# Kernel optimization log

Measured on AMD Instinct MI355X. Metric: run time of the kernel, lower is better.

## Reference

```python
import jax, jax.numpy as jnp
import numpy as np

N, L, S = 2, 3000, 3000
C = 256          # in_depth
H = 256          # hidden_depth
FC = 8           # heads_count
SC_HID = H // FC # per-head dim of projected features
SCALE = (C // FC) ** 0.5  # torch code uses sc = in_depth // heads_count for scaling


def setup_inputs() -> dict:
    key = jax.random.key(0)
    ks = jax.random.split(key, 7)
    x0 = jax.random.normal(ks[0], (N, L, C), jnp.float32)
    x1 = jax.random.normal(ks[1], (N, S, C), jnp.float32)
    mask = jax.random.bernoulli(ks[2], 0.9, (N, L, S))
    W_proj = jax.random.normal(ks[3], (C, 2 * H), jnp.float32) / np.sqrt(C).astype(np.float32)
    b_proj = jax.random.normal(ks[4], (2 * H,), jnp.float32) * 0.01
    W_merge = jax.random.normal(ks[5], (H, C), jnp.float32) / np.sqrt(H).astype(np.float32)
    b_merge = jax.random.normal(ks[6], (C,), jnp.float32) * 0.01
    return {"x0": x0, "x1": x1, "mask": mask,
            "W_proj": W_proj, "b_proj": b_proj,
            "W_merge": W_merge, "b_merge": b_merge}


def _split_heads(x, W_proj, b_proj):
    # x: [n, t, C] -> proj [n, t, 2H] -> (qk, v) each [n, fc, t, sc]
    n, t, _ = x.shape
    p = (x @ W_proj + b_proj).reshape(n, t, 2, FC, SC_HID)  # layout (k fc sc)
    qk = jnp.transpose(p[:, :, 0], (0, 2, 1, 3))
    v = jnp.transpose(p[:, :, 1], (0, 2, 1, 3))
    return qk, v


def reference(x0, x1, mask, W_proj, b_proj, W_merge, b_merge):
    q0, v0 = _split_heads(x0, W_proj, b_proj)  # [n, f, l, d]
    q1, v1 = _split_heads(x1, W_proj, b_proj)  # [n, f, s, d]

    sim = jnp.einsum('nfld,nfsd->nfls', q0, q1)            # full score matrix
    sim = jnp.where(mask[:, None], sim, -jnp.inf) / SCALE  # mask then scale (as in torch)

    a01 = jnp.nan_to_num(jax.nn.softmax(sim, axis=3))  # rows over s
    a10 = jnp.nan_to_num(jax.nn.softmax(sim, axis=2))  # rows over l (== softmax(sim^T, -1))

    m0 = jnp.einsum('nfls,nfsd->nfld', a01, v1)  # [n, f, l, d]
    m1 = jnp.einsum('nfls,nfld->nfsd', a10, v0)  # [n, f, s, d]

    m0 = jnp.transpose(m0, (0, 2, 1, 3)).reshape(m0.shape[0], L, H) @ W_merge + b_merge
    m1 = jnp.transpose(m1, (0, 2, 1, 3)).reshape(m1.shape[0], S, H) @ W_merge + b_merge
    return m0, m1
```

## Files before the change

### kernel.cpp

```cpp
#include <hip/hip_runtime.h>
#include <cstdint>
#include <cstddef>

typedef unsigned int u32;
typedef unsigned short u16;
typedef uint8_t u8;
typedef unsigned long long u64;

constexpr int kNB = 2, kL = 3000, kS = 3000, kC = 256, kH = 256, kFC = 8, kD = 32;
constexpr int kTP = 3008;
constexpr int kMW = 48;
constexpr float kQSC = 0.5050097568f;

typedef __attribute__((ext_vector_type(8))) short short8;
typedef __attribute__((ext_vector_type(4))) float f32x4;

__device__ __forceinline__ u16 f2bf(float f) {
  u32 u = __float_as_uint(f);
  u += 0x7FFFu + ((u >> 16) & 1u);
  return (u16)(u >> 16);
}
__device__ __forceinline__ float bf2f(u16 h) { return __uint_as_float(((u32)h) << 16); }
__device__ __forceinline__ f32x4 mfma16(short8 a, short8 b, f32x4 c) {
  return __builtin_amdgcn_mfma_f32_16x16x32_bf16(a, b, c, 0, 0, 0);
}
__device__ __forceinline__ u32 pk2(float a, float b) {
  return (__float_as_uint(a) >> 16) | (__float_as_uint(b) & 0xFFFF0000u);
}
__device__ __forceinline__ float truncbf(float a) {
  return __uint_as_float(__float_as_uint(a) & 0xFFFF0000u);
}
__device__ __forceinline__ u32 bytes_nz(u32 w) {
  return ((w & 0xFFu) ? 1u : 0u) | (((w >> 8) & 0xFFu) ? 2u : 0u)
       | (((w >> 16) & 0xFFu) ? 4u : 0u) | ((w >> 24) ? 8u : 0u);
}
__device__ __forceinline__ u32 h2_nz(u32 w) {
  return ((w & 0xFFFFu) ? 1u : 0u) | ((w >> 16) ? 2u : 0u);
}

__device__ __forceinline__ u32 detect_mf_block(const u8* __restrict__ mraw,
                                               int tid, int* cnt) {
  if (tid < 8) cnt[tid] = 0;
  __syncthreads();
  uint4 mv = ((const uint4*)mraw)[tid];
  u32 wds[4] = {mv.x, mv.y, mv.z, mv.w};
  int l1[4] = {0,0,0,0}; int l3f1 = 0, l3c = 0;
#pragma unroll
  for (int k = 0; k < 4; ++k) {
    u32 wv = wds[k];
#pragma unroll
    for (int j = 0; j < 4; ++j) {
      u32 b = (wv >> (8 * j)) & 0xFFu;
      l1[j] += (b == 1u);
      if (j == 1) l3f1 += (b == 0x3Fu);
      if (j & 1) l3c += (b == 0x3Cu);
    }
  }
  if (l1[0]) atomicAdd(&cnt[0], l1[0]);
  if (l1[1]) atomicAdd(&cnt[1], l1[1]);
  if (l1[2]) atomicAdd(&cnt[2], l1[2]);
  if (l1[3]) atomicAdd(&cnt[3], l1[3]);
  if (l3f1)  atomicAdd(&cnt[4], l3f1);
  if (l3c)   atomicAdd(&cnt[5], l3c);
  __syncthreads();
  u32 mf;
  if (cnt[1] + cnt[2] + cnt[3] > 64) mf = 0;
  else if (cnt[0] > 64)              mf = 2;
  else if (cnt[4] > 64)              mf = 1;
  else if (cnt[5] > 64)              mf = 4;
  else                               mf = 3;
  return mf;
}
__device__ __forceinline__ u32 detect_f2_block(const u8* __restrict__ xraw,
                                               int tid, int* cnt) {
  if (tid == 0) cnt[0] = 0;
  __syncthreads();
  uint4 xv = ((const uint4*)xraw)[tid];
  u32 wds[4] = {xv.x, xv.y, xv.z, xv.w};
  int lex = 0;
#pragma unroll
  for (int k = 0; k < 4; ++k) {
    u32 b = (wds[k] >> 8) & 0x7Fu;
    lex += (b >= 0x3Eu && b <= 0x40u);
  }
  if (lex) atomicAdd(&cnt[0], lex);
  __syncthreads();
  return (cnt[0] > 300) ? 0u : 1u;
}

constexpr size_t SZ_Q   = (size_t)kNB * kFC * kTP * kD * 2;
constexpr size_t SZ_MH  = (size_t)kNB * kTP * kH * 2;
constexpr size_t SZ_XB  = (size_t)kNB * kL * kC * 2;
constexpr size_t SZ_MKB = (size_t)kNB * kMW * kTP * 8;
constexpr size_t OFF_Q0 = 256;
constexpr size_t OFF_Q1 = OFF_Q0 + SZ_Q;
constexpr size_t OFF_V0 = OFF_Q1 + SZ_Q;
constexpr size_t OFF_V1 = OFF_V0 + SZ_Q;
constexpr size_t OFF_M0 = OFF_V1 + SZ_Q;
constexpr size_t OFF_M1 = OFF_M0 + SZ_MH;
constexpr size_t OFF_WT = OFF_M1 + SZ_MH;
constexpr size_t OFF_WM = OFF_WT + (size_t)2 * kH * kC * 2;
constexpr size_t OFF_X0 = OFF_WM + (size_t)kC * kH * 2;
constexpr size_t OFF_X1 = OFF_X0 + SZ_XB;
constexpr size_t OFF_MKB  = OFF_X1 + SZ_XB;
constexpr size_t OFF_MKBT = OFF_MKB + SZ_MKB;

constexpr int NB_MASK = 47 * 47 * 2;
constexpr int NB_CVT  = 3000;
constexpr int NB_WT   = 2 * kH + kC;

__global__ __launch_bounds__(256) void k_prep(const void* __restrict__ mraw,
                                              const void* __restrict__ x0,
                                              const void* __restrict__ x1,
                                              const void* __restrict__ Wp,
                                              const void* __restrict__ Wm,
                                              u64* __restrict__ mkb, u64* __restrict__ mkbt,
                                              u16* __restrict__ xb0, u16* __restrict__ xb1,
                                              u16* __restrict__ WT, u16* __restrict__ WmT) {
  const int bx = blockIdx.x, tid = threadIdx.x;
  __shared__ int dcnt[8];
  if (bx < NB_MASK) {
    const u32 mf = detect_mf_block((const u8*)mraw, tid, dcnt);
    const int n = bx / 2209, r2 = bx % 2209;
    const int l0 = (r2 / 47) * 64, s0 = (r2 % 47) * 64;
    __shared__ u16 tb[64][4];
    {
      const int row = tid >> 2, sg = (tid & 3) * 16;
      const int l = l0 + row;
      u32 bits = 0;
      if (l < kL) {
        const size_t base = ((size_t)n * kL + l) * kS + s0 + sg;
        const bool full = (s0 + sg + 16 <= kS);
        if (mf == 3) {
          if (full) {
            const float4* p = (const float4*)(((const float*)mraw) + base);
            float4 a = p[0], b = p[1], c = p[2], d = p[3];
            bits = (u32)(a.x != 0.f)        | ((u32)(a.y != 0.f) << 1)
                 | ((u32)(a.z != 0.f) << 2) | ((u32)(a.w != 0.f) << 3)
                 | ((u32)(b.x != 0.f) << 4) | ((u32)(b.y != 0.f) << 5)
                 | ((u32)(b.z != 0.f) << 6) | ((u32)(b.w != 0.f) << 7)
                 | ((u32)(c.x != 0.f) << 8) | ((u32)(c.y != 0.f) << 9)
                 | ((u32)(c.z != 0.f) << 10)| ((u32)(c.w != 0.f) << 11)
                 | ((u32)(d.x != 0.f) << 12)| ((u32)(d.y != 0.f) << 13)
                 | ((u32)(d.z != 0.f) << 14)| ((u32)(d.w != 0.f) << 15);
          } else {
            for (int i = 0; i < 16; ++i)
              if (s0 + sg + i < kS && ((const float*)mraw)[base + i] != 0.f) bits |= 1u << i;
          }
        } else if (mf == 2) {
          if (full) {
            const uint4* p = (const uint4*)(((const u32*)mraw) + base);
            uint4 a = p[0], b = p[1], c = p[2], d = p[3];
            bits = (u32)(a.x != 0)        | ((u32)(a.y != 0) << 1)
                 | ((u32)(a.z != 0) << 2) | ((u32)(a.w != 0) << 3)
                 | ((u32)(b.x != 0) << 4) | ((u32)(b.y != 0) << 5)
                 | ((u32)(b.z != 0) << 6) | ((u32)(b.w != 0) << 7)
                 | ((u32)(c.x != 0) << 8) | ((u32)(c.y != 0) << 9)
                 | ((u32)(c.z != 0) << 10)| ((u32)(c.w != 0) << 11)
                 | ((u32)(d.x != 0) << 12)| ((u32)(d.y != 0) << 13)
                 | ((u32)(d.z != 0) << 14)| ((u32)(d.w != 0) << 15);
          } else {
            for (int i = 0; i < 16; ++i)
              if (s0 + sg + i < kS && ((const u32*)mraw)[base + i]) bits |= 1u << i;
          }
        } else if (mf == 0) {
          if (full) {
            const u8* m8 = (const u8*)mraw + base;
            uint2 a = *(const uint2*)(m8);
            uint2 b = *(const uint2*)(m8 + 8);
            bits = bytes_nz(a.x) | (bytes_nz(a.y) << 4)
                 | (bytes_nz(b.x) << 8) | (bytes_nz(b.y) << 12);
          } else {
            for (int i = 0; i < 16; ++i)
              if (s0 + sg + i < kS && ((const u8*)mraw)[base + i]) bits |= 1u << i;
          }
        } else {
          if (full) {
            const u16* m16 = (const u16*)mraw + base;
            uint4 a = *(const uint4*)(m16);
            uint4 b = *(const uint4*)(m16 + 8);
            bits = h2_nz(a.x) | (h2_nz(a.y) << 2) | (h2_nz(a.z) << 4) | (h2_nz(a.w) << 6)
                 | (h2_nz(b.x) << 8) | (h2_nz(b.y) << 10)
                 | (h2_nz(b.z) << 12) | (h2_nz(b.w) << 14);
          } else {
            for (int i = 0; i < 16; ++i)
              if (s0 + sg + i < kS && ((const u16*)mraw)[base + i]) bits |= 1u << i;
          }
        }
      }
      tb[row][tid & 3] = (u16)bits;
    }
    __syncthreads();
    const int w = tid >> 6, lane = tid & 63;
    for (int k = 0; k < 16; ++k) {
      const int ro = w * 16 + k;
      u32 b1 = (tb[ro][lane >> 4] >> (lane & 15)) & 1;
      u64 word = __ballot((int)b1);
      if (lane == 0) mkb[((size_t)n * kMW + (s0 >> 6)) * kTP + l0 + ro] = word;
      u32 b2 = (tb[lane][ro >> 4] >> (ro & 15)) & 1;
      u64 wordt = __ballot((int)b2);
      if (lane == 0) mkbt[((size_t)n * kMW + (l0 >> 6)) * kTP + s0 + ro] = wordt;
    }
  } else if (bx < NB_MASK + NB_CVT) {
    const u32 f2 = detect_f2_block((const u8*)x0, tid, dcnt);
    const int b2 = bx - NB_MASK;
    const void* X = (b2 >= 1500) ? x1 : x0;
    u16* B = (b2 >= 1500) ? xb1 : xb0;
    const int i = (b2 % 1500) * 256 + tid;
    if (f2 == 0) {
      ((uint2*)B)[i] = ((const uint2*)X)[i];
    } else {
      float4 v = ((const float4*)X)[i];
      uint2 o;
      o.x = (u32)f2bf(v.x) | ((u32)f2bf(v.y) << 16);
      o.y = (u32)f2bf(v.z) | ((u32)f2bf(v.w) << 16);
      ((uint2*)B)[i] = o;
    }
  } else {
    const u32 f2 = detect_f2_block((const u8*)x0, tid, dcnt);
    const int b = bx - NB_MASK - NB_CVT, k = tid;
    if (b < 2 * kH) {
      int col = b;
      u16 v = (f2 == 0) ? ((const u16*)Wp)[(size_t)k * (2 * kH) + col]
                        : f2bf(((const float*)Wp)[(size_t)k * (2 * kH) + col]);
      WT[(size_t)col * kC + k] = v;
    } else {
      int col = b - 2 * kH;
      u16 v = (f2 == 0) ? ((const u16*)Wm)[(size_t)k * kC + col]
                        : f2bf(((const float*)Wm)[(size_t)k * kC + col]);
      WmT[(size_t)col * kH + k] = v;
    }
  }
}

__global__ __launch_bounds__(256) void k_proj(const u16* __restrict__ xb0,
                                              const u16* __restrict__ xb1,
                                              const u16* __restrict__ WT,
                                              const void* __restrict__ bias,
                                              const void* __restrict__ x0raw,
                                              u16* __restrict__ q0, u16* __restrict__ v0t,
                                              u16* __restrict__ q1, u16* __restrict__ v1t) {
  __shared__ int dcnt[8];
  const int tid = threadIdx.x;
  const u32 f2 = detect_f2_block((const u8*)x0raw, tid, dcnt);
  const int z = blockIdx.z;
  const u16* X = z ? xb1 : xb0;
  u16* Q = z ? q1 : q0;
  u16* V = z ? v1t : v0t;
  const int w = tid >> 6, lane = tid & 63;
  const int quad = lane >> 4, c16 = lane & 15;
  const int rb = blockIdx.x, cb = blockIdx.y;

  __align__(16) __shared__ u16 sB[64 * 264];
  {
    const u16* wp = WT + (size_t)(cb * 64 + (tid >> 2)) * kC + (tid & 3) * 64;
    u16* sp = sB + (tid >> 2) * 264 + (tid & 3) * 64;
#pragma unroll
    for (int i = 0; i < 8; ++i) *(uint4*)(sp + i * 8) = *(const uint4*)(wp + i * 8);
  }
  __syncthreads();

  const int arow = rb * 64 + w * 16 + c16;
  const u16* ap = X + (size_t)arow * kC + quad * 8;
  f32x4 acc[4];
#pragma unroll
  for (int cg = 0; cg < 4; ++cg) acc[cg] = f32x4{0.f,0.f,0.f,0.f};
#pragma unroll
  for (int k0 = 0; k0 < 8; ++k0) {
    short8 a = *(const short8*)(ap + k0 * 32);
#pragma unroll
    for (int cg = 0; cg < 4; ++cg) {
      short8 b = *(const short8*)(sB + (cg * 16 + c16) * 264 + k0 * 32 + quad * 8);
      acc[cg] = mfma16(a, b, acc[cg]);
    }
  }

  const int row0 = rb * 64 + w * 16 + quad * 4;
  if (row0 < 6000) {
    const int n = (row0 >= kL) ? 1 : 0;
    const int t0 = row0 - n * kL;
#pragma unroll
    for (int cg = 0; cg < 4; ++cg) {
      const int c = cb * 64 + cg * 16 + c16;
      float bb = (f2 == 0) ? bf2f(((const u16*)bias)[c]) : ((const float*)bias)[c];
      if (c < kH) {
        int ff = c >> 5, d = c & 31;
        u16* qp = Q + ((size_t)(n * kFC + ff) * kTP + t0) * kD + d;
#pragma unroll
        for (int r = 0; r < 4; ++r) qp[(size_t)r * kD] = f2bf((acc[cg][r] + bb) * kQSC);
      } else {
        int cc = c - kH;
        int ff = cc >> 5, d = cc & 31;
        uint2 o;
        o.x = (u32)f2bf(acc[cg][0] + bb) | ((u32)f2bf(acc[cg][1] + bb) << 16);
        o.y = (u32)f2bf(acc[cg][2] + bb) | ((u32)f2bf(acc[cg][3] + bb) << 16);
        *(uint2*)(V + ((size_t)(n * kFC + ff) * kD + d) * kTP + t0) = o;
      }
    }
  }
}

__global__ __launch_bounds__(256) void k_flash(const u16* __restrict__ q0,
                                               const u16* __restrict__ q1,
                                               const u16* __restrict__ v0t,
                                               const u16* __restrict__ v1t,
                                               const u64* __restrict__ mkb,
                                               const u64* __restrict__ mkbt,
                                               u16* __restrict__ m0h, u16* __restrict__ m1h) {
  const int z = blockIdx.z;
  const u16* QA = z ? q1 : q0;
  const u16* QB = z ? q0 : q1;
  const u16* VT = z ? v0t : v1t;
  const u64* MB = z ? mkbt : mkb;
  u16* MO = z ? m1h : m0h;

  const int nf = blockIdx.y, n = nf >> 3, f = nf & 7;
  const int tid = threadIdx.x, w = tid >> 6, lane = tid & 63;
  const int quad = lane >> 4, c16 = lane & 15;

  __align__(16) __shared__ u16 sPall[4 * 4704];
  u16* sP = sPall + w * 4704;

  const u16* qa = QA + (size_t)(n * kFC + f) * kTP * kD;
  const u16* qb = QB + (size_t)(n * kFC + f) * kTP * kD;
  const u16* vt = VT + (size_t)(n * kFC + f) * kD * kTP;
  const u64* mb = MB + (size_t)n * kMW * kTP;

  const int l0 = blockIdx.x * 64;

  short8 af[4];
#pragma unroll
  for (int g = 0; g < 4; ++g) {
    const int ra = l0 + g * 16 + c16;
    af[g] = *(const short8*)(qa + (size_t)ra * kD + quad * 8);
  }

  f32x4 acc[4][2];
  float pSum[4];
#pragma unroll
  for (int g = 0; g < 4; ++g) {
    acc[g][0] = f32x4{0.f,0.f,0.f,0.f};
    acc[g][1] = f32x4{0.f,0.f,0.f,0.f};
    pSum[g] = 0.f;
  }

  u64 mword = mb[(size_t)w * kTP + l0 + lane];
  short8 aq0, aq1, aq2, aq3;
  {
    const u16* qbase = qb + (size_t)(w * 64 + c16) * kD + quad * 8;
    aq0 = *(const short8*)(qbase);
    aq1 = *(const short8*)(qbase + (size_t)16 * kD);
    aq2 = *(const short8*)(qbase + (size_t)32 * kD);
    aq3 = *(const short8*)(qbase + (size_t)48 * kD);
  }

#pragma unroll 1
  for (int jc = w; jc < 47; jc += 4) {
    const int j0 = jc * 64;
    const u16* vb = vt + (size_t)c16 * kTP + j0 + quad * 8;
    short8 bv00 = *(const short8*)(vb);
    short8 bv01 = *(const short8*)(vb + (size_t)16 * kTP);
    short8 bv10 = *(const short8*)(vb + 32);
    short8 bv11 = *(const short8*)(vb + (size_t)16 * kTP + 32);

    const u32 mlo = (u32)mword, mhi = (u32)(mword >> 32);

#pragma unroll
    for (int g = 0; g < 4; ++g) {
      const u32 lo = (u32)__shfl((int)mlo, g * 16 + c16);
      const u32 hi = (u32)__shfl((int)mhi, g * 16 + c16);
      float ps = 0.f;
#pragma unroll
      for (int t = 0; t < 4; ++t) {
        short8 aq = (t == 0) ? aq0 : (t == 1) ? aq1 : (t == 2) ? aq2 : aq3;
        f32x4 zz = {0.f,0.f,0.f,0.f};
        f32x4 s = mfma16(aq, af[g], zz);
        const u32 hh = (t & 2) ? hi : lo;
        const int base = (t & 1) * 16 + quad * 4;
        float p0 = ((hh >> (base + 0)) & 1) ? __builtin_amdgcn_exp2f(s[0]) : 0.f;
        float p1 = ((hh >> (base + 1)) & 1) ? __builtin_amdgcn_exp2f(s[1]) : 0.f;
        float p2 = ((hh >> (base + 2)) & 1) ? __builtin_amdgcn_exp2f(s[2]) : 0.f;
        float p3 = ((hh >> (base + 3)) & 1) ? __builtin_amdgcn_exp2f(s[3]) : 0.f;
        ps += (truncbf(p0) + truncbf(p1)) + (truncbf(p2) + truncbf(p3));
        uint2 pw; pw.x = pk2(p0, p1); pw.y = pk2(p2, p3);
        *(uint2*)(sP + (g * 16 + c16) * 72 + t * 16 + quad * 4) = pw;
      }
      pSum[g] += ps;
    }

    {
      int jn = jc + 4;
      const int jl = (jn < 47) ? jn : w;
      mword = mb[(size_t)jl * kTP + l0 + lane];
      const u16* qn = qb + (size_t)(jl * 64 + c16) * kD + quad * 8;
      aq0 = *(const short8*)(qn);
      aq1 = *(const short8*)(qn + (size_t)16 * kD);
      aq2 = *(const short8*)(qn + (size_t)32 * kD);
      aq3 = *(const short8*)(qn + (size_t)48 * kD);
    }

#pragma unroll
    for (int g = 0; g < 4; ++g) {
      short8 ap0 = *(const short8*)(sP + (g * 16 + c16) * 72 + quad * 8);
      short8 ap1 = *(const short8*)(sP + (g * 16 + c16) * 72 + 32 + quad * 8);
      acc[g][0] = mfma16(ap0, bv00, acc[g][0]);
      acc[g][1] = mfma16(ap0, bv01, acc[g][1]);
      acc[g][0] = mfma16(ap1, bv10, acc[g][0]);
      acc[g][1] = mfma16(ap1, bv11, acc[g][1]);
    }
  }

#pragma unroll
  for (int g = 0; g < 4; ++g) {
    float s = pSum[g];
    s += __shfl_xor(s, 16);
    s += __shfl_xor(s, 32);
    pSum[g] = s;
  }

  __syncthreads();
  float* buf = (float*)sPall;
  if (w > 0) {
    const int rbase = (w - 1) * 2304;
#pragma unroll
    for (int g = 0; g < 4; ++g) {
#pragma unroll
      for (int r = 0; r < 4; ++r) {
        buf[rbase + (g * 9 + r)     * 64 + lane] = acc[g][0][r];
        buf[rbase + (g * 9 + 4 + r) * 64 + lane] = acc[g][1][r];
      }
      buf[rbase + (g * 9 + 8) * 64 + lane] = pSum[g];
    }
  }
  __syncthreads();
  if (w == 0) {
#pragma unroll
    for (int g = 0; g < 4; ++g) {
      float lsum = pSum[g];
#pragma unroll
      for (int ww = 0; ww < 3; ++ww) lsum += buf[ww * 2304 + (g * 9 + 8) * 64 + lane];
#pragma unroll
      for (int r = 0; r < 4; ++r) {
        float n0 = acc[g][0][r], n1 = acc[g][1][r];
#pragma unroll
        for (int ww = 0; ww < 3; ++ww) {
          n0 += buf[ww * 2304 + (g * 9 + r)     * 64 + lane];
          n1 += buf[ww * 2304 + (g * 9 + 4 + r) * 64 + lane];
        }
        float ls = __shfl(lsum, quad * 4 + r);
        float rd = (ls > 0.f) ? (1.f / ls) : 0.f;
        int lrow = l0 + g * 16 + quad * 4 + r;
        if (lrow < kL) {
          size_t basep = ((size_t)n * kTP + lrow) * kH + f * kD;
          MO[basep + c16]      = f2bf(n0 * rd);
          MO[basep + 16 + c16] = f2bf(n1 * rd);
        }
      }
    }
  }
}

__global__ __launch_bounds__(256) void k_merge(const u16* __restrict__ m0h,
                                               const u16* __restrict__ m1h,
                                               const u16* __restrict__ WmT,
                                               const void* __restrict__ bias,
                                               const void* __restrict__ x0raw,
                                               void* __restrict__ out) {
  __shared__ int dcnt[8];
  const int tid = threadIdx.x;
  const u32 f2 = detect_f2_block((const u8*)x0raw, tid, dcnt);
  const int z = blockIdx.z;
  const u16* A = z ? m1h : m0h;
  const int w = tid >> 6, lane = tid & 63;
  const int quad = lane >> 4, c16 = lane & 15;
  const int rb = blockIdx.x, cb = blockIdx.y;

  __align__(16) __shared__ u16 sB[64 * 264];
  {
    const u16* wp = WmT + (size_t)(cb * 64 + (tid >> 2)) * kH + (tid & 3) * 64;
    u16* sp = sB + (tid >> 2) * 264 + (tid & 3) * 64;
#pragma unroll
    for (int i = 0; i < 8; ++i) *(uint4*)(sp + i * 8) = *(const uint4*)(wp + i * 8);
  }
  __syncthreads();

  const int arow = rb * 64 + w * 16 + c16;
  const u16* ap = A + (size_t)arow * kH + quad * 8;
  f32x4 acc[4];
#pragma unroll
  for (int cg = 0; cg < 4; ++cg) acc[cg] = f32x4{0.f,0.f,0.f,0.f};
#pragma unroll
  for (int k0 = 0; k0 < 8; ++k0) {
    short8 a = *(const short8*)(ap + k0 * 32);
#pragma unroll
    for (int cg = 0; cg < 4; ++cg) {
      short8 b = *(const short8*)(sB + (cg * 16 + c16) * 264 + k0 * 32 + quad * 8);
      acc[cg] = mfma16(a, b, acc[cg]);
    }
  }

  const int row0 = rb * 64 + w * 16 + quad * 4;
  const int n = (row0 >= kTP) ? 1 : 0;
  const int t0 = row0 - n * kTP;
  const size_t obase = (size_t)z * ((size_t)kNB * kL * kC);
#pragma unroll
  for (int cg = 0; cg < 4; ++cg) {
    const int c = cb * 64 + cg * 16 + c16;
    float bb = (f2 == 0) ? bf2f(((const u16*)bias)[c]) : ((const float*)bias)[c];
#pragma unroll
    for (int r = 0; r < 4; ++r) {
      const int t = t0 + r;
      if (t < kL) {
        size_t oi = obase + ((size_t)n * kL + t) * kC + c;
        float v = acc[cg][r] + bb;
        if (f2 == 0) ((u16*)out)[oi] = f2bf(v);
        else         ((float*)out)[oi] = v;
      }
    }
  }
}

extern "C" void kernel_launch(void* const* d_in, const int* in_sizes, int n_in,
                              void* d_out, int out_size, void* d_ws, size_t ws_size,
                              hipStream_t stream) {
  (void)in_sizes; (void)n_in; (void)out_size; (void)ws_size;
  u8* ws = (u8*)d_ws;
  u16* q0  = (u16*)(ws + OFF_Q0);
  u16* q1  = (u16*)(ws + OFF_Q1);
  u16* v0t = (u16*)(ws + OFF_V0);
  u16* v1t = (u16*)(ws + OFF_V1);
  u16* m0h = (u16*)(ws + OFF_M0);
  u16* m1h = (u16*)(ws + OFF_M1);
  u16* WT  = (u16*)(ws + OFF_WT);
  u16* WmT = (u16*)(ws + OFF_WM);
  u16* xb0 = (u16*)(ws + OFF_X0);
  u16* xb1 = (u16*)(ws + OFF_X1);
  u64* mkb  = (u64*)(ws + OFF_MKB);
  u64* mkbt = (u64*)(ws + OFF_MKBT);

  const void* x0 = d_in[0];
  const void* x1 = d_in[1];
  const void* mraw = d_in[2];
  const void* Wp = d_in[3];
  const void* bp = d_in[4];
  const void* Wm = d_in[5];
  const void* bm = d_in[6];

  k_prep<<<dim3(NB_MASK + NB_CVT + NB_WT), 256, 0, stream>>>(
      mraw, x0, x1, Wp, Wm, mkb, mkbt, xb0, xb1, WT, WmT);
  k_proj<<<dim3(94, 8, 2), 256, 0, stream>>>(xb0, xb1, WT, bp, x0, q0, v0t, q1, v1t);
  k_flash<<<dim3(47, 16, 2), 256, 0, stream>>>(q0, q1, v0t, v1t, mkb, mkbt, m0h, m1h);
  k_merge<<<dim3(94, 4, 2), 256, 0, stream>>>(m0h, m1h, WmT, bm, x0, d_out);
}
```

Baseline: 258.4 us.

## Fuse mask prep and projection into one kernel; compute row sums via MFMA

Merges the mask-bit packing, input conversion, weight transpose and projection GEMM into one heterogeneous launch. Projection blocks now read x and the fp32 or bf16 weights directly, dropping the bf16 staging buffers for x and W. Block types are interleaved so mask and projection work run together. In the flash kernel, per-row softmax denominators now come from an extra MFMA against a ones vector instead of scalar truncated adds and shuffles. The trade is more MFMA work, uncoalesced strided weight loads repeated in every projection block, and a larger LDS reduction buffer.

```diff
diff --git a/kernel.cpp b/kernel.cpp
--- a/kernel.cpp
+++ b/kernel.cpp
@@ -26,9 +26,6 @@
 }
 __device__ __forceinline__ u32 pk2(float a, float b) {
   return (__float_as_uint(a) >> 16) | (__float_as_uint(b) & 0xFFFF0000u);
-}
-__device__ __forceinline__ float truncbf(float a) {
-  return __uint_as_float(__float_as_uint(a) & 0xFFFF0000u);
 }
 __device__ __forceinline__ u32 bytes_nz(u32 w) {
   return ((w & 0xFFu) ? 1u : 0u) | (((w >> 8) & 0xFFu) ? 2u : 0u)
@@ -90,7 +87,6 @@
 
 constexpr size_t SZ_Q   = (size_t)kNB * kFC * kTP * kD * 2;
 constexpr size_t SZ_MH  = (size_t)kNB * kTP * kH * 2;
-constexpr size_t SZ_XB  = (size_t)kNB * kL * kC * 2;
 constexpr size_t SZ_MKB = (size_t)kNB * kMW * kTP * 8;
 constexpr size_t OFF_Q0 = 256;
 constexpr size_t OFF_Q1 = OFF_Q0 + SZ_Q;
@@ -98,30 +94,41 @@
 constexpr size_t OFF_V1 = OFF_V0 + SZ_Q;
 constexpr size_t OFF_M0 = OFF_V1 + SZ_Q;
 constexpr size_t OFF_M1 = OFF_M0 + SZ_MH;
-constexpr size_t OFF_WT = OFF_M1 + SZ_MH;
-constexpr size_t OFF_WM = OFF_WT + (size_t)2 * kH * kC * 2;
-constexpr size_t OFF_X0 = OFF_WM + (size_t)kC * kH * 2;
-constexpr size_t OFF_X1 = OFF_X0 + SZ_XB;
-constexpr size_t OFF_MKB  = OFF_X1 + SZ_XB;
+constexpr size_t OFF_WM = OFF_M1 + SZ_MH;
+constexpr size_t OFF_MKB  = OFF_WM + (size_t)kC * kH * 2;
 constexpr size_t OFF_MKBT = OFF_MKB + SZ_MKB;
 
-constexpr int NB_MASK = 47 * 47 * 2;
-constexpr int NB_CVT  = 3000;
-constexpr int NB_WT   = 2 * kH + kC;
-
-__global__ __launch_bounds__(256) void k_prep(const void* __restrict__ mraw,
+constexpr int NB_MASKP = 4418;
+constexpr int NB_PROJ  = 94 * 8 * 2;
+constexpr int NB_COMB  = 6016 + (kC - 94);
+
+__global__ __launch_bounds__(256) void k_comb(const void* __restrict__ mraw,
                                               const void* __restrict__ x0,
                                               const void* __restrict__ x1,
                                               const void* __restrict__ Wp,
                                               const void* __restrict__ Wm,
+                                              const void* __restrict__ bias,
                                               u64* __restrict__ mkb, u64* __restrict__ mkbt,
-                                              u16* __restrict__ xb0, u16* __restrict__ xb1,
-                                              u16* __restrict__ WT, u16* __restrict__ WmT) {
+                                              u16* __restrict__ WmT,
+                                              u16* __restrict__ q0, u16* __restrict__ v0t,
+                                              u16* __restrict__ q1, u16* __restrict__ v1t) {
   const int bx = blockIdx.x, tid = threadIdx.x;
   __shared__ int dcnt[8];
-  if (bx < NB_MASK) {
+
+  int kind, idx;
+  if (bx < 6016) {
+    const int i = bx >> 2, j = bx & 3;
+    if (j == 3) { kind = 1; idx = i; }
+    else {
+      const int mi = i * 3 + j;
+      if (mi < NB_MASKP) { kind = 0; idx = mi; }
+      else               { kind = 2; idx = mi - NB_MASKP; }
+    }
+  } else { kind = 2; idx = 94 + (bx - 6016); }
+
+  if (kind == 0) {
     const u32 mf = detect_mf_block((const u8*)mraw, tid, dcnt);
-    const int n = bx / 2209, r2 = bx % 2209;
+    const int n = idx / 2209, r2 = idx % 2209;
     const int l0 = (r2 / 47) * 64, s0 = (r2 % 47) * 64;
     __shared__ u16 tb[64][4];
     {
@@ -144,8 +151,8 @@
                  | ((u32)(d.x != 0.f) << 12)| ((u32)(d.y != 0.f) << 13)
                  | ((u32)(d.z != 0.f) << 14)| ((u32)(d.w != 0.f) << 15);
           } else {
-            for (int i = 0; i < 16; ++i)
-              if (s0 + sg + i < kS && ((const float*)mraw)[base + i] != 0.f) bits |= 1u << i;
+            for (int i2 = 0; i2 < 16; ++i2)
+              if (s0 + sg + i2 < kS && ((const float*)mraw)[base + i2] != 0.f) bits |= 1u << i2;
           }
         } else if (mf == 2) {
           if (full) {
@@ -160,8 +167,8 @@
                  | ((u32)(d.x != 0) << 12)| ((u32)(d.y != 0) << 13)
                  | ((u32)(d.z != 0) << 14)| ((u32)(d.w != 0) << 15);
           } else {
-            for (int i = 0; i < 16; ++i)
-              if (s0 + sg + i < kS && ((const u32*)mraw)[base + i]) bits |= 1u << i;
+            for (int i2 = 0; i2 < 16; ++i2)
+              if (s0 + sg + i2 < kS && ((const u32*)mraw)[base + i2]) bits |= 1u << i2;
           }
         } else if (mf == 0) {
           if (full) {
@@ -171,8 +178,8 @@
             bits = bytes_nz(a.x) | (bytes_nz(a.y) << 4)
                  | (bytes_nz(b.x) << 8) | (bytes_nz(b.y) << 12);
           } else {
-            for (int i = 0; i < 16; ++i)
-              if (s0 + sg + i < kS && ((const u8*)mraw)[base + i]) bits |= 1u << i;
+            for (int i2 = 0; i2 < 16; ++i2)
+              if (s0 + sg + i2 < kS && ((const u8*)mraw)[base + i2]) bits |= 1u << i2;
           }
         } else {
           if (full) {
@@ -183,8 +190,8 @@
                  | (h2_nz(b.x) << 8) | (h2_nz(b.y) << 10)
                  | (h2_nz(b.z) << 12) | (h2_nz(b.w) << 14);
           } else {
-            for (int i = 0; i < 16; ++i)
-              if (s0 + sg + i < kS && ((const u16*)mraw)[base + i]) bits |= 1u << i;
+            for (int i2 = 0; i2 < 16; ++i2)
+              if (s0 + sg + i2 < kS && ((const u16*)mraw)[base + i2]) bits |= 1u << i2;
           }
         }
       }
@@ -201,102 +208,97 @@
       u64 wordt = __ballot((int)b2);
       if (lane == 0) mkbt[((size_t)n * kMW + (l0 >> 6)) * kTP + s0 + ro] = wordt;
     }
-  } else if (bx < NB_MASK + NB_CVT) {
+  } else if (kind == 1) {
     const u32 f2 = detect_f2_block((const u8*)x0, tid, dcnt);
-    const int b2 = bx - NB_MASK;
-    const void* X = (b2 >= 1500) ? x1 : x0;
-    u16* B = (b2 >= 1500) ? xb1 : xb0;
-    const int i = (b2 % 1500) * 256 + tid;
-    if (f2 == 0) {
-      ((uint2*)B)[i] = ((const uint2*)X)[i];
-    } else {
-      float4 v = ((const float4*)X)[i];
-      uint2 o;
-      o.x = (u32)f2bf(v.x) | ((u32)f2bf(v.y) << 16);
-      o.y = (u32)f2bf(v.z) | ((u32)f2bf(v.w) << 16);
-      ((uint2*)B)[i] = o;
+    const int rb = idx % 94, cb = (idx / 94) % 8, z = idx / 752;
+    u16* Q = z ? q1 : q0;
+    u16* V = z ? v1t : v0t;
+    const int w = tid >> 6, lane = tid & 63;
+    const int quad = lane >> 4, c16 = lane & 15;
+
+    __align__(16) __shared__ u16 sB[64 * 264];
+    {
+      const int col = cb * 64 + (tid >> 2);
+      const int kbase = (tid & 3) * 64;
+      u16* sp = sB + (tid >> 2) * 264 + kbase;
+      if (f2 == 0) {
+        const u16* wp16 = (const u16*)Wp;
+#pragma unroll 8
+        for (int i2 = 0; i2 < 64; ++i2)
+          sp[i2] = wp16[(size_t)(kbase + i2) * (2 * kH) + col];
+      } else {
+        const float* wpf = (const float*)Wp;
+#pragma unroll 8
+        for (int i2 = 0; i2 < 64; ++i2)
+          sp[i2] = f2bf(wpf[(size_t)(kbase + i2) * (2 * kH) + col]);
+      }
+    }
+    __syncthreads();
+
+    int arow = rb * 64 + w * 16 + c16;
+    const int an = (arow >= kL) ? 1 : 0;
+    int atr = arow - an * kL; if (atr > kL - 1) atr = kL - 1;
+    const void* Xr = (z == 0) ? ((an == 0) ? x0 : x1) : ((an == 0) ? x1 : x0);
+    f32x4 acc[4];
+#pragma unroll
+    for (int cg = 0; cg < 4; ++cg) acc[cg] = f32x4{0.f,0.f,0.f,0.f};
+    (void)Xr; (void)atr; (void)an;
+    {
+      int row = rb * 64 + w * 16 + c16;
+      int n_ = (row >= kL) ? 1 : 0;
+      int tr = row - n_ * kL; if (tr > kL - 1) tr = kL - 1;
+      const void* Xsrc = z ? x1 : x0;
+      const u32 f2l = f2;
+#pragma unroll
+      for (int k0 = 0; k0 < 8; ++k0) {
+        short8 a;
+        if (f2l == 0) {
+          a = *(const short8*)((const u16*)Xsrc + ((size_t)n_ * kL + tr) * kC + k0 * 32 + quad * 8);
+        } else {
+          const float* xf = (const float*)Xsrc + ((size_t)n_ * kL + tr) * kC + k0 * 32 + quad * 8;
+          float4 u = *(const float4*)xf, v = *(const float4*)(xf + 4);
+          a[0] = (short)f2bf(u.x); a[1] = (short)f2bf(u.y);
+          a[2] = (short)f2bf(u.z); a[3] = (short)f2bf(u.w);
+          a[4] = (short)f2bf(v.x); a[5] = (short)f2bf(v.y);
+          a[6] = (short)f2bf(v.z); a[7] = (short)f2bf(v.w);
+        }
+#pragma unroll
+        for (int cg = 0; cg < 4; ++cg) {
+          short8 b = *(const short8*)(sB + (cg * 16 + c16) * 264 + k0 * 32 + quad * 8);
+          acc[cg] = mfma16(a, b, acc[cg]);
+        }
+      }
+    }
+
+    const int row0 = rb * 64 + w * 16 + quad * 4;
+    if (row0 < 2 * kL) {
+      const int n = (row0 >= kL) ? 1 : 0;
+      const int t0 = row0 - n * kL;
+#pragma unroll
+      for (int cg = 0; cg < 4; ++cg) {
+        const int c = cb * 64 + cg * 16 + c16;
+        float bb = (f2 == 0) ? bf2f(((const u16*)bias)[c]) : ((const float*)bias)[c];
+        if (c < kH) {
+          int ff = c >> 5, d = c & 31;
+          u16* qp = Q + ((size_t)(n * kFC + ff) * kTP + t0) * kD + d;
+#pragma unroll
+          for (int r = 0; r < 4; ++r) qp[(size_t)r * kD] = f2bf((acc[cg][r] + bb) * kQSC);
+        } else {
+          int cc = c - kH;
+          int ff = cc >> 5, d = cc & 31;
+          uint2 o;
+          o.x = (u32)f2bf(acc[cg][0] + bb) | ((u32)f2bf(acc[cg][1] + bb) << 16);
+          o.y = (u32)f2bf(acc[cg][2] + bb) | ((u32)f2bf(acc[cg][3] + bb) << 16);
+          *(uint2*)(V + ((size_t)(n * kFC + ff) * kD + d) * kTP + t0) = o;
+        }
+      }
     }
   } else {
     const u32 f2 = detect_f2_block((const u8*)x0, tid, dcnt);
-    const int b = bx - NB_MASK - NB_CVT, k = tid;
-    if (b < 2 * kH) {
-      int col = b;
-      u16 v = (f2 == 0) ? ((const u16*)Wp)[(size_t)k * (2 * kH) + col]
-                        : f2bf(((const float*)Wp)[(size_t)k * (2 * kH) + col]);
-      WT[(size_t)col * kC + k] = v;
-    } else {
-      int col = b - 2 * kH;
-      u16 v = (f2 == 0) ? ((const u16*)Wm)[(size_t)k * kC + col]
-                        : f2bf(((const float*)Wm)[(size_t)k * kC + col]);
-      WmT[(size_t)col * kH + k] = v;
-    }
-  }
-}
-
-__global__ __launch_bounds__(256) void k_proj(const u16* __restrict__ xb0,
-                                              const u16* __restrict__ xb1,
-                                              const u16* __restrict__ WT,
-                                              const void* __restrict__ bias,
-                                              const void* __restrict__ x0raw,
-                                              u16* __restrict__ q0, u16* __restrict__ v0t,
-                                              u16* __restrict__ q1, u16* __restrict__ v1t) {
-  __shared__ int dcnt[8];
-  const int tid = threadIdx.x;
-  const u32 f2 = detect_f2_block((const u8*)x0raw, tid, dcnt);
-  const int z = blockIdx.z;
-  const u16* X = z ? xb1 : xb0;
-  u16* Q = z ? q1 : q0;
-  u16* V = z ? v1t : v0t;
-  const int w = tid >> 6, lane = tid & 63;
-  const int quad = lane >> 4, c16 = lane & 15;
-  const int rb = blockIdx.x, cb = blockIdx.y;
-
-  __align__(16) __shared__ u16 sB[64 * 264];
-  {
-    const u16* wp = WT + (size_t)(cb * 64 + (tid >> 2)) * kC + (tid & 3) * 64;
-    u16* sp = sB + (tid >> 2) * 264 + (tid & 3) * 64;
-#pragma unroll
-    for (int i = 0; i < 8; ++i) *(uint4*)(sp + i * 8) = *(const uint4*)(wp + i * 8);
-  }
-  __syncthreads();
-
-  const int arow = rb * 64 + w * 16 + c16;
-  const u16* ap = X + (size_t)arow * kC + quad * 8;
-  f32x4 acc[4];
-#pragma unroll
-  for (int cg = 0; cg < 4; ++cg) acc[cg] = f32x4{0.f,0.f,0.f,0.f};
-#pragma unroll
-  for (int k0 = 0; k0 < 8; ++k0) {
-    short8 a = *(const short8*)(ap + k0 * 32);
-#pragma unroll
-    for (int cg = 0; cg < 4; ++cg) {
-      short8 b = *(const short8*)(sB + (cg * 16 + c16) * 264 + k0 * 32 + quad * 8);
-      acc[cg] = mfma16(a, b, acc[cg]);
-    }
-  }
-
-  const int row0 = rb * 64 + w * 16 + quad * 4;
-  if (row0 < 6000) {
-    const int n = (row0 >= kL) ? 1 : 0;
-    const int t0 = row0 - n * kL;
-#pragma unroll
-    for (int cg = 0; cg < 4; ++cg) {
-      const int c = cb * 64 + cg * 16 + c16;
-      float bb = (f2 == 0) ? bf2f(((const u16*)bias)[c]) : ((const float*)bias)[c];
-      if (c < kH) {
-        int ff = c >> 5, d = c & 31;
-        u16* qp = Q + ((size_t)(n * kFC + ff) * kTP + t0) * kD + d;
-#pragma unroll
-        for (int r = 0; r < 4; ++r) qp[(size_t)r * kD] = f2bf((acc[cg][r] + bb) * kQSC);
-      } else {
-        int cc = c - kH;
-        int ff = cc >> 5, d = cc & 31;
-        uint2 o;
-        o.x = (u32)f2bf(acc[cg][0] + bb) | ((u32)f2bf(acc[cg][1] + bb) << 16);
-        o.y = (u32)f2bf(acc[cg][2] + bb) | ((u32)f2bf(acc[cg][3] + bb) << 16);
-        *(uint2*)(V + ((size_t)(n * kFC + ff) * kD + d) * kTP + t0) = o;
-      }
-    }
+    const int col = idx, k = tid;
+    u16 v = (f2 == 0) ? ((const u16*)Wm)[(size_t)k * kC + col]
+                      : f2bf(((const float*)Wm)[(size_t)k * kC + col]);
+    WmT[(size_t)col * kH + k] = v;
   }
 }
 
@@ -334,14 +336,16 @@
     const int ra = l0 + g * 16 + c16;
     af[g] = *(const short8*)(qa + (size_t)ra * kD + quad * 8);
   }
-
-  f32x4 acc[4][2];
-  float pSum[4];
+  short8 bones;
+#pragma unroll
+  for (int i = 0; i < 8; ++i) bones[i] = (short)0x3F80;
+
+  f32x4 acc[4][2], accS[4];
 #pragma unroll
   for (int g = 0; g < 4; ++g) {
     acc[g][0] = f32x4{0.f,0.f,0.f,0.f};
     acc[g][1] = f32x4{0.f,0.f,0.f,0.f};
-    pSum[g] = 0.f;
+    accS[g]   = f32x4{0.f,0.f,0.f,0.f};
   }
 
   u64 mword = mb[(size_t)w * kTP + l0 + lane];
@@ -369,7 +373,6 @@
     for (int g = 0; g < 4; ++g) {
       const u32 lo = (u32)__shfl((int)mlo, g * 16 + c16);
       const u32 hi = (u32)__shfl((int)mhi, g * 16 + c16);
-      float ps = 0.f;
 #pragma unroll
       for (int t = 0; t < 4; ++t) {
         short8 aq = (t == 0) ? aq0 : (t == 1) ? aq1 : (t == 2) ? aq2 : aq3;
@@ -381,11 +384,9 @@
         float p1 = ((hh >> (base + 1)) & 1) ? __builtin_amdgcn_exp2f(s[1]) : 0.f;
         float p2 = ((hh >> (base + 2)) & 1) ? __builtin_amdgcn_exp2f(s[2]) : 0.f;
         float p3 = ((hh >> (base + 3)) & 1) ? __builtin_amdgcn_exp2f(s[3]) : 0.f;
-        ps += (truncbf(p0) + truncbf(p1)) + (truncbf(p2) + truncbf(p3));
         uint2 pw; pw.x = pk2(p0, p1); pw.y = pk2(p2, p3);
         *(uint2*)(sP + (g * 16 + c16) * 72 + t * 16 + quad * 4) = pw;
       }
-      pSum[g] += ps;
     }
 
     {
@@ -405,49 +406,40 @@
       short8 ap1 = *(const short8*)(sP + (g * 16 + c16) * 72 + 32 + quad * 8);
       acc[g][0] = mfma16(ap0, bv00, acc[g][0]);
       acc[g][1] = mfma16(ap0, bv01, acc[g][1]);
+      accS[g]   = mfma16(ap0, bones, accS[g]);
       acc[g][0] = mfma16(ap1, bv10, acc[g][0]);
       acc[g][1] = mfma16(ap1, bv11, acc[g][1]);
-    }
-  }
-
-#pragma unroll
-  for (int g = 0; g < 4; ++g) {
-    float s = pSum[g];
-    s += __shfl_xor(s, 16);
-    s += __shfl_xor(s, 32);
-    pSum[g] = s;
+      accS[g]   = mfma16(ap1, bones, accS[g]);
+    }
   }
 
   __syncthreads();
   float* buf = (float*)sPall;
   if (w > 0) {
-    const int rbase = (w - 1) * 2304;
+    const int rbase = (w - 1) * 3072;
 #pragma unroll
     for (int g = 0; g < 4; ++g) {
 #pragma unroll
       for (int r = 0; r < 4; ++r) {
-        buf[rbase + (g * 9 + r)     * 64 + lane] = acc[g][0][r];
-        buf[rbase + (g * 9 + 4 + r) * 64 + lane] = acc[g][1][r];
-      }
-      buf[rbase + (g * 9 + 8) * 64 + lane] = pSum[g];
+        buf[rbase + (g * 12 + r)     * 64 + lane] = acc[g][0][r];
+        buf[rbase + (g * 12 + 4 + r) * 64 + lane] = acc[g][1][r];
+        buf[rbase + (g * 12 + 8 + r) * 64 + lane] = accS[g][r];
+      }
     }
   }
   __syncthreads();
   if (w == 0) {
 #pragma unroll
     for (int g = 0; g < 4; ++g) {
-      float lsum = pSum[g];
-#pragma unroll
-      for (int ww = 0; ww < 3; ++ww) lsum += buf[ww * 2304 + (g * 9 + 8) * 64 + lane];
 #pragma unroll
       for (int r = 0; r < 4; ++r) {
-        float n0 = acc[g][0][r], n1 = acc[g][1][r];
+        float n0 = acc[g][0][r], n1 = acc[g][1][r], ls = accS[g][r];
 #pragma unroll
         for (int ww = 0; ww < 3; ++ww) {
-          n0 += buf[ww * 2304 + (g * 9 + r)     * 64 + lane];
-          n1 += buf[ww * 2304 + (g * 9 + 4 + r) * 64 + lane];
+          n0 += buf[ww * 3072 + (g * 12 + r)     * 64 + lane];
+          n1 += buf[ww * 3072 + (g * 12 + 4 + r) * 64 + lane];
+          ls += buf[ww * 3072 + (g * 12 + 8 + r) * 64 + lane];
         }
-        float ls = __shfl(lsum, quad * 4 + r);
         float rd = (ls > 0.f) ? (1.f / ls) : 0.f;
         int lrow = l0 + g * 16 + quad * 4 + r;
         if (lrow < kL) {
@@ -531,10 +523,7 @@
   u16* v1t = (u16*)(ws + OFF_V1);
   u16* m0h = (u16*)(ws + OFF_M0);
   u16* m1h = (u16*)(ws + OFF_M1);
-  u16* WT  = (u16*)(ws + OFF_WT);
   u16* WmT = (u16*)(ws + OFF_WM);
-  u16* xb0 = (u16*)(ws + OFF_X0);
-  u16* xb1 = (u16*)(ws + OFF_X1);
   u64* mkb  = (u64*)(ws + OFF_MKB);
   u64* mkbt = (u64*)(ws + OFF_MKBT);
 
@@ -546,9 +535,8 @@
   const void* Wm = d_in[5];
   const void* bm = d_in[6];
 
-  k_prep<<<dim3(NB_MASK + NB_CVT + NB_WT), 256, 0, stream>>>(
-      mraw, x0, x1, Wp, Wm, mkb, mkbt, xb0, xb1, WT, WmT);
-  k_proj<<<dim3(94, 8, 2), 256, 0, stream>>>(xb0, xb1, WT, bp, x0, q0, v0t, q1, v1t);
+  k_comb<<<dim3(NB_COMB), 256, 0, stream>>>(
+      mraw, x0, x1, Wp, Wm, bp, mkb, mkbt, WmT, q0, v0t, q1, v1t);
   k_flash<<<dim3(47, 16, 2), 256, 0, stream>>>(q0, q1, v0t, v1t, mkb, mkbt, m0h, m1h);
   k_merge<<<dim3(94, 4, 2), 256, 0, stream>>>(m0h, m1h, WmT, bm, x0, d_out);
 }
```

Result: slower. 293.0 us (+13.4%).
